# Performance work log

Measured on AMD Instinct MI355X. Metric: run time of the kernel, lower is better.

## Reference

```python
import jax, jax.numpy as jnp
import numpy as np

NUM_HEADS = 8
NUM_LEVELS = 4
NUM_POINTS = 8
SPATIAL_SHAPES = np.array([[92, 160], [46, 80], [23, 40], [12, 20]], dtype=np.int64)


def _bilinear_sample(val_hw, loc, Hl, Wl):
    """val_hw: (bs, heads, H*W, d); loc: (bs, nq, heads, P, 2) in [0,1].
    Matches torch grid_sample(bilinear, zeros padding, align_corners=False)
    applied to grid = 2*loc - 1, i.e. pixel coords x = loc_x*W - 0.5.
    Returns (bs, heads, nq, P, d)."""
    x = loc[..., 0] * Wl - 0.5
    y = loc[..., 1] * Hl - 0.5
    x0 = jnp.floor(x)
    y0 = jnp.floor(y)
    wx = (x - x0).transpose(0, 2, 1, 3)  # (bs, heads, nq, P)
    wy = (y - y0).transpose(0, 2, 1, 3)
    x0i = x0.astype(jnp.int32).transpose(0, 2, 1, 3)
    y0i = y0.astype(jnp.int32).transpose(0, 2, 1, 3)

    def gather(ix, iy):
        valid = ((ix >= 0) & (ix < Wl) & (iy >= 0) & (iy < Hl)).astype(val_hw.dtype)
        idx = jnp.clip(iy, 0, Hl - 1) * Wl + jnp.clip(ix, 0, Wl - 1)  # (bs,heads,nq,P)
        b, h, nq, P = idx.shape
        g = jnp.take_along_axis(val_hw, idx.reshape(b, h, nq * P, 1), axis=2)
        return g.reshape(b, h, nq, P, -1) * valid[..., None]

    return (gather(x0i, y0i) * ((1 - wx) * (1 - wy))[..., None]
            + gather(x0i + 1, y0i) * (wx * (1 - wy))[..., None]
            + gather(x0i, y0i + 1) * ((1 - wx) * wy)[..., None]
            + gather(x0i + 1, y0i + 1) * (wx * wy)[..., None])


def setup_inputs() -> dict:
    key = jax.random.key(0)
    ks = jax.random.split(key, 10)
    C = 256
    bs, nq = 2, 10000
    nv = int((SPATIAL_SHAPES[:, 0] * SPATIAL_SHAPES[:, 1]).sum())  # 19560
    s = 1.0 / np.sqrt(C)
    return {
        "query": jax.random.normal(ks[0], (bs, nq, C), dtype=jnp.float32),
        "value": jax.random.normal(ks[1], (bs, nv, C), dtype=jnp.float32),
        "reference_points": jax.random.uniform(ks[2], (bs, nq, 4, 2), dtype=jnp.float32),
        "spatial_shapes": SPATIAL_SHAPES,
        "W_value": jax.random.normal(ks[3], (C, C), dtype=jnp.float32) * s,
        "b_value": jnp.zeros((C,), dtype=jnp.float32),
        "W_off": jax.random.normal(ks[4], (C, NUM_HEADS * NUM_LEVELS * NUM_POINTS * 2), dtype=jnp.float32) * 0.01,
        "b_off": jax.random.normal(ks[5], (NUM_HEADS * NUM_LEVELS * NUM_POINTS * 2,), dtype=jnp.float32) * 0.1,
        "W_attn": jax.random.normal(ks[6], (C, NUM_HEADS * NUM_LEVELS * NUM_POINTS), dtype=jnp.float32) * s,
        "b_attn": jnp.zeros((NUM_HEADS * NUM_LEVELS * NUM_POINTS,), dtype=jnp.float32),
    }


def reference(query, value, reference_points, spatial_shapes,
              W_value, b_value, W_off, b_off, W_attn, b_attn):
    bs, nq, C = query.shape
    NH, NL, NP = NUM_HEADS, NUM_LEVELS, NUM_POINTS
    d = C // NH
    Z = reference_points.shape[2]  # num_Z_anchors
    shapes_np = np.asarray(spatial_shapes)  # static host-side shapes

    # value / offset / attention projections
    v = (value @ W_value + b_value).reshape(bs, -1, NH, d)
    off = (query @ W_off + b_off).reshape(bs, nq, NH, NL, NP, 2)
    attn = jax.nn.softmax((query @ W_attn + b_attn).reshape(bs, nq, NH, NL * NP), axis=-1)
    attn = attn.reshape(bs, nq, NH, NL, NP)

    # normalize offsets by (W, H) per level and add to reference points
    norm = jnp.stack([spatial_shapes[:, 1], spatial_shapes[:, 0]], -1).astype(query.dtype)  # (NL, 2)
    off = off / norm[None, None, None, :, None, :]
    off = off.reshape(bs, nq, NH, NL, NP // Z, Z, 2)
    loc = reference_points[:, :, None, None, None, :, :] + off  # (bs,nq,NH,NL,NP//Z,Z,2)
    loc = loc.reshape(bs, nq, NH, NL, NP, 2)

    out = jnp.zeros((bs, NH, nq, d), dtype=query.dtype)
    start = 0
    for l in range(NL):
        Hl, Wl = int(shapes_np[l, 0]), int(shapes_np[l, 1])
        v_l = v[:, start:start + Hl * Wl].transpose(0, 2, 1, 3)  # (bs, NH, H*W, d)
        start += Hl * Wl
        sampled = _bilinear_sample(v_l, loc[:, :, :, l], Hl, Wl)  # (bs,NH,nq,NP,d)
        out = out + jnp.einsum('bhqpd,bqhp->bhqd', sampled, attn[:, :, :, l])
    return out.transpose(0, 2, 1, 3).reshape(bs, nq, NH * d)
```

## Files before the change

### kernel.cpp

```cpp
#include <hip/hip_runtime.h>
#include <math.h>

#define NH 8
#define NL 4
#define NP 8
#define CDIM 256
#define NQ 10000
#define BS 2
#define NV 19560

__constant__ int LVL_H[NL]     = {92, 46, 23, 12};
__constant__ int LVL_W[NL]     = {160, 80, 40, 20};
__constant__ int LVL_START[NL] = {0, 14720, 18400, 19320};

typedef __attribute__((ext_vector_type(8))) short short8;
typedef __attribute__((ext_vector_type(4))) float f32x4;
typedef __attribute__((ext_vector_type(2))) _Float16 half2v;
typedef __attribute__((ext_vector_type(4))) _Float16 half4v;

__device__ __forceinline__ unsigned short f2bf(float f) {
    unsigned int u = __float_as_uint(f);
    u += 0x7fffu + ((u >> 16) & 1u);
    return (unsigned short)(u >> 16);
}

__device__ __forceinline__ unsigned cvt_pk_bf16(float lo, float hi) {
    unsigned r;
    asm("v_cvt_pk_bf16_f32 %0, %1, %2" : "=v"(r) : "v"(lo), "v"(hi));
    return r;
}

__device__ __forceinline__ unsigned f2h_dup(float f) {
    const unsigned short h = __builtin_bit_cast(unsigned short, (_Float16)f);
    return (unsigned)h | ((unsigned)h << 16);
}

__device__ __forceinline__ void glds16(const void* g, void* l) {
    __builtin_amdgcn_global_load_lds(
        (const __attribute__((address_space(1))) unsigned*)g,
        (__attribute__((address_space(3))) unsigned*)l, 16, 0, 0);
}

__global__ __launch_bounds__(256) void prep_all(
    const float* __restrict__ query,
    const float* __restrict__ Wv,
    const float* __restrict__ Woff, const float* __restrict__ boff,
    const float* __restrict__ Wattn, const float* __restrict__ battn,
    unsigned short* __restrict__ querybf,
    unsigned short* __restrict__ BvalT, unsigned short* __restrict__ BcatT,
    float* __restrict__ biascat)
{
    const int bid = blockIdx.x;
    const int t   = threadIdx.x;
    if (bid < 5000) {
        const int i = bid * 256 + t;
        const float4 f = ((const float4*)query)[i];
        ushort4 o;
        o.x = f2bf(f.x); o.y = f2bf(f.y); o.z = f2bf(f.z); o.w = f2bf(f.w);
        ((ushort4*)querybf)[i] = o;
    } else {
        const int n = bid - 5000;
        if (n < 256) {
            BvalT[n * 256 + t] = f2bf(Wv[t * 256 + n]);
        } else if (n < 1024) {
            const int m = n - 256;
            const float v = (m < 512) ? Woff[t * 512 + m]
                                      : Wattn[t * 256 + (m - 512)];
            BcatT[m * 256 + t] = f2bf(v);
        } else {
            #pragma unroll
            for (int s = 0; s < 3; s++) {
                const int i = s * 256 + t;
                biascat[i] = (i < 512) ? boff[i] : battn[i - 512];
            }
        }
    }
}

__global__ __launch_bounds__(256) void gemm_all(
    const float* __restrict__ valueF,
    const unsigned short* __restrict__ BvalT,
    const float* __restrict__ b_value, _Float16* __restrict__ vproj,
    const unsigned short* __restrict__ querybf,
    const unsigned short* __restrict__ BcatT,
    const float* __restrict__ biascat, _Float16* __restrict__ offcat)
{
    __shared__ short8 Asl[512];
    __shared__ short8 Bsl[512];

    const int bid = blockIdx.x;
    const bool modeV = bid < 612;

    const unsigned short* Bt;
    const float* bias;
    int M, N, rowBase, colBase;
    if (modeV) {
        Bt = BvalT; bias = b_value;
        M = BS * NV; N = 256;
        rowBase = (bid >> 1) * 128; colBase = (bid & 1) * 128;
    } else {
        const int b2 = bid - 612;
        Bt = BcatT; bias = biascat;
        M = BS * NQ; N = 768;
        rowBase = (b2 / 6) * 128; colBase = (b2 % 6) * 128;
    }

    const int t = threadIdx.x;
    const int w  = t >> 6;
    const int l  = t & 63;
    const int wm = (w >> 1) * 64;
    const int wn = (w & 1) * 64;
    const int row16 = l & 15;
    const int kg    = l >> 4;

    const int r0 = t >> 2;
    const int m_ = t & 3;
    const int cs = (m_ - (r0 >> 1)) & 3;

    short8* aw0 = &Asl[(w << 6)];
    short8* aw1 = &Asl[256 + (w << 6)];
    short8* bw0 = &Bsl[(w << 6)];
    short8* bw1 = &Bsl[256 + (w << 6)];

    const int arow0 = min(rowBase + r0, M - 1);
    const int arow1 = min(rowBase + r0 + 64, M - 1);
    const int brow0 = colBase + r0;
    const int brow1 = brow0 + 64;

    f32x4 acc[4][4] = {};

    for (int k0 = 0; k0 < 256; k0 += 32) {
        const int kc = k0 + cs * 8;
        glds16(Bt + (size_t)brow0 * 256 + kc, bw0);
        glds16(Bt + (size_t)brow1 * 256 + kc, bw1);
        if (modeV) {
            #pragma unroll
            for (int jj = 0; jj < 2; jj++) {
                const int ar = jj ? arow1 : arow0;
                const float* ap = valueF + (size_t)ar * 256 + kc;
                const float4 f0 = *(const float4*)ap;
                const float4 f1 = *(const float4*)(ap + 4);
                uint4 pk;
                pk.x = cvt_pk_bf16(f0.x, f0.y);
                pk.y = cvt_pk_bf16(f0.z, f0.w);
                pk.z = cvt_pk_bf16(f1.x, f1.y);
                pk.w = cvt_pk_bf16(f1.z, f1.w);
                Asl[jj * 256 + t] = __builtin_bit_cast(short8, pk);
            }
        } else {
            glds16(querybf + (size_t)arow0 * 256 + kc, aw0);
            glds16(querybf + (size_t)arow1 * 256 + kc, aw1);
        }
        __syncthreads();

        short8 af[4], bfr[4];
        #pragma unroll
        for (int i = 0; i < 4; i++) {
            const int r = wm + i * 16 + row16;
            af[i] = Asl[r * 4 + ((kg + (r >> 1)) & 3)];
        }
        #pragma unroll
        for (int j = 0; j < 4; j++) {
            const int r = wn + j * 16 + row16;
            bfr[j] = Bsl[r * 4 + ((kg + (r >> 1)) & 3)];
        }
        #pragma unroll
        for (int i = 0; i < 4; i++)
            #pragma unroll
            for (int j = 0; j < 4; j++)
                acc[i][j] = __builtin_amdgcn_mfma_f32_16x16x32_bf16(
                    bfr[j], af[i], acc[i][j], 0, 0, 0);
        __syncthreads();
    }

    const int m16 = l & 15;
    const int q4  = (l >> 4) * 4;
    #pragma unroll
    for (int i = 0; i < 4; i++) {
        const int row = rowBase + wm + i * 16 + m16;
        if (row >= M) continue;
        #pragma unroll
        for (int j = 0; j < 4; j++) {
            const int col0 = colBase + wn + j * 16 + q4;
            const float4 bv = *(const float4*)&bias[col0];
            half4v o;
            o[0] = (_Float16)(acc[i][j][0] + bv.x);
            o[1] = (_Float16)(acc[i][j][1] + bv.y);
            o[2] = (_Float16)(acc[i][j][2] + bv.z);
            o[3] = (_Float16)(acc[i][j][3] + bv.w);
            _Float16* dst;
            if (modeV) {
                const int b   = (row >= NV) ? 1 : 0;
                const int pix = row - b * NV;
                const int h   = col0 >> 5;
                const int ch  = col0 & 31;
                dst = vproj + ((size_t)(b * NH + h) * NV + pix) * 32 + ch;
            } else {
                dst = offcat + (size_t)row * 768 + col0;
            }
            *(half4v*)dst = o;
        }
    }
}

__global__ __launch_bounds__(256, 8) void sample_kernel(
    const _Float16* __restrict__ vproj,
    const _Float16* __restrict__ offcat,
    const float* __restrict__ refpts,
    float* __restrict__ out)
{
    const int bid = blockIdx.x;
    const int h   = bid & 7;
    const int g   = bid >> 3;
    const int b   = g & 1;
    const int q0  = (g >> 1) * 8;
    const int t   = threadIdx.x;

    __shared__ uint2 desc[8 * 144];

    const int qi = t >> 5, j = t & 31;
    const int qrow = b * NQ + q0 + qi;

    {
        const int lv = j >> 3, p = j & 7;

        const float logit = (float)offcat[(size_t)qrow * 768 + 512 + h * 32 + j];
        const float e = __expf(logit);
        float ssum = e;
        #pragma unroll
        for (int s = 16; s > 0; s >>= 1) ssum += __shfl_xor(ssum, s, 32);
        const float aw = e / ssum;

        const int Wl = LVL_W[lv], Hl = LVL_H[lv], st = LVL_START[lv];
        const uint oxy = *(const uint*)(offcat + (size_t)qrow * 768 + h * 64 + j * 2);
        const float offx = (float)__builtin_bit_cast(half2v, oxy)[0];
        const float offy = (float)__builtin_bit_cast(half2v, oxy)[1];

        const int z = p & 3;
        const float rx = refpts[((size_t)qrow * 4 + z) * 2];
        const float ry = refpts[((size_t)qrow * 4 + z) * 2 + 1];

        const float x = fmaf(rx, (float)Wl, offx) - 0.5f;
        const float y = fmaf(ry, (float)Hl, offy) - 0.5f;
        const float x0f = floorf(x), y0f = floorf(y);
        const float wx = x - x0f, wy = y - y0f;
        const int x0 = (int)x0f, y0 = (int)y0f;

        const int xb = min(max(x0, 0), Wl - 2);
        const float wl = (x0 >= 0 && x0 < Wl)          ? (1.f - wx) : 0.f;
        const float wr = (x0 + 1 >= 0 && x0 + 1 < Wl)  ? wx         : 0.f;
        const float wA = (x0 == xb) ? wl : ((x0 + 1 == xb) ? wr : 0.f);
        const float wB = (x0 == xb) ? wr : ((x0 == xb + 1) ? wl : 0.f);

        const int i16 = j >> 1;
        const int gA0 = qi * 144 + (((j & 1) * 2) * 2) * 18 + i16;

        #pragma unroll
        for (int r = 0; r < 2; r++) {
            const int yy = y0 + r;
            const float rwv = (yy >= 0 && yy < Hl)
                            ? (r ? wy : (1.f - wy)) * aw : 0.f;
            const int iy = min(max(yy, 0), Hl - 1);
            const unsigned base = (unsigned)((st + iy * Wl + xb) * 64);
            const int gb = gA0 + r * 2 * 18;
            desc[gb]      = make_uint2(base,      f2h_dup(wA * rwv));
            desc[gb + 18] = make_uint2(base + 64, f2h_dup(wB * rwv));
        }
    }
    __syncthreads();

    const int lane = t & 31;
    const int grp  = lane >> 3;
    const int pix  = (lane >> 2) & 1;
    const int chq  = lane & 3;

    const char* slab = (const char*)(vproj + (size_t)(b * NH + h) * NV * 32);
    const unsigned laneoff = (unsigned)(chq * 16);
    const uint4* dp = (const uint4*)&desc[qi * 144 + (grp * 2 + pix) * 18];

    half2v a0 = {}, a1 = {}, a2 = {}, a3 = {};
    #pragma unroll
    for (int half = 0; half < 2; half++) {
        uint4 d4[4];
        #pragma unroll
        for (int u2 = 0; u2 < 4; u2++) d4[u2] = dp[half * 4 + u2];
        uint4 v[8];
        #pragma unroll
        for (int u2 = 0; u2 < 4; u2++) {
            v[u2 * 2]     = *(const uint4*)(slab + (d4[u2].x + laneoff));
            v[u2 * 2 + 1] = *(const uint4*)(slab + (d4[u2].z + laneoff));
        }
        __builtin_amdgcn_sched_barrier(0);
        #pragma unroll
        for (int u2 = 0; u2 < 4; u2++) {
            const half2v w0 = __builtin_bit_cast(half2v, d4[u2].y);
            a0 += w0 * __builtin_bit_cast(half2v, v[u2 * 2].x);
            a1 += w0 * __builtin_bit_cast(half2v, v[u2 * 2].y);
            a2 += w0 * __builtin_bit_cast(half2v, v[u2 * 2].z);
            a3 += w0 * __builtin_bit_cast(half2v, v[u2 * 2].w);
            const half2v w1 = __builtin_bit_cast(half2v, d4[u2].w);
            a0 += w1 * __builtin_bit_cast(half2v, v[u2 * 2 + 1].x);
            a1 += w1 * __builtin_bit_cast(half2v, v[u2 * 2 + 1].y);
            a2 += w1 * __builtin_bit_cast(half2v, v[u2 * 2 + 1].z);
            a3 += w1 * __builtin_bit_cast(half2v, v[u2 * 2 + 1].w);
        }
    }

    #pragma unroll
    for (int s = 4; s <= 16; s <<= 1) {
        a0 += __builtin_bit_cast(half2v,
              __shfl_xor(__builtin_bit_cast(unsigned, a0), s, 32));
        a1 += __builtin_bit_cast(half2v,
              __shfl_xor(__builtin_bit_cast(unsigned, a1), s, 32));
        a2 += __builtin_bit_cast(half2v,
              __shfl_xor(__builtin_bit_cast(unsigned, a2), s, 32));
        a3 += __builtin_bit_cast(half2v,
              __shfl_xor(__builtin_bit_cast(unsigned, a3), s, 32));
    }

    if ((lane & 0x1C) == 0) {
        float* op = out + (size_t)qrow * 256 + h * 32 + chq * 8;
        *(float4*)op = make_float4((float)a0[0], (float)a0[1],
                                   (float)a1[0], (float)a1[1]);
        *(float4*)(op + 4) = make_float4((float)a2[0], (float)a2[1],
                                         (float)a3[0], (float)a3[1]);
    }
}

extern "C" void kernel_launch(void* const* d_in, const int* in_sizes, int n_in,
                              void* d_out, int out_size, void* d_ws, size_t ws_size,
                              hipStream_t stream)
{
    const float* query   = (const float*)d_in[0];
    const float* value   = (const float*)d_in[1];
    const float* refpts  = (const float*)d_in[2];
    const float* W_value = (const float*)d_in[4];
    const float* b_value = (const float*)d_in[5];
    const float* W_off   = (const float*)d_in[6];
    const float* b_off   = (const float*)d_in[7];
    const float* W_attn  = (const float*)d_in[8];
    const float* b_attn  = (const float*)d_in[9];

    char* ws = (char*)d_ws;
    _Float16*       vproj   = (_Float16*)(ws);
    unsigned short* querybf = (unsigned short*)(ws + 20029440);
    _Float16*       offcat  = (_Float16*)(ws + 30269440);
    unsigned short* BvalT   = (unsigned short*)(ws + 60989440);
    unsigned short* BcatT   = (unsigned short*)(ws + 61120512);
    float*          biascat = (float*)(ws + 61513728);

    const dim3 blk(256);

    prep_all<<<dim3(6025), blk, 0, stream>>>(
        query, W_value, W_off, b_off, W_attn, b_attn,
        querybf, BvalT, BcatT, biascat);

    gemm_all<<<dim3(1554), blk, 0, stream>>>(
        value, BvalT, b_value, vproj,
        querybf, BcatT, biascat, offcat);

    sample_kernel<<<dim3(BS * NQ), blk, 0, stream>>>(
        vproj, offcat, refpts, (float*)d_out);
}
```

Before: 211.9 us.

## Double-buffer GEMM LDS tiles, remap blocks across XCDs, relax sample occupancy

The fused GEMM kernel now double-buffers its A and B shared-memory tiles, issuing the next k-step's global-to-LDS loads before computing on the current tile. It replaces __syncthreads with explicit waitcnt plus s_barrier so loads overlap with MFMA work. Block IDs are remapped so that consecutive logical tiles land on the same XCD, improving L2 reuse. The sample kernel's launch bound drops from 8 to 6 blocks per CU, which allows more registers per thread. The hand-written vmcnt counts are fragile and could cause races if the compiler's ordering of memory operations differs from what they assume.

```diff
diff --git a/kernel.cpp b/kernel.cpp
--- a/kernel.cpp
+++ b/kernel.cpp
@@ -85,10 +85,15 @@
     const unsigned short* __restrict__ BcatT,
     const float* __restrict__ biascat, _Float16* __restrict__ offcat)
 {
-    __shared__ short8 Asl[512];
-    __shared__ short8 Bsl[512];
-
-    const int bid = blockIdx.x;
+    __shared__ short8 Asl[2][512];
+    __shared__ short8 Bsl[2][512];
+
+    const int orig = blockIdx.x;
+    const int xcd  = orig & 7, lid = orig >> 3;
+    const int q_   = 1554 >> 3, r_ = 1554 & 7;
+    const int bid  = (xcd < r_ ? xcd * (q_ + 1)
+                               : r_ * (q_ + 1) + (xcd - r_) * q_) + lid;
+
     const bool modeV = bid < 612;
 
     const unsigned short* Bt;
@@ -117,10 +122,7 @@
     const int m_ = t & 3;
     const int cs = (m_ - (r0 >> 1)) & 3;
 
-    short8* aw0 = &Asl[(w << 6)];
-    short8* aw1 = &Asl[256 + (w << 6)];
-    short8* bw0 = &Bsl[(w << 6)];
-    short8* bw1 = &Bsl[256 + (w << 6)];
+    const int wb = w << 6;
 
     const int arow0 = min(rowBase + r0, M - 1);
     const int arow1 = min(rowBase + r0 + 64, M - 1);
@@ -129,40 +131,62 @@
 
     f32x4 acc[4][4] = {};
 
-    for (int k0 = 0; k0 < 256; k0 += 32) {
-        const int kc = k0 + cs * 8;
-        glds16(Bt + (size_t)brow0 * 256 + kc, bw0);
-        glds16(Bt + (size_t)brow1 * 256 + kc, bw1);
+    #define STAGE_Q(s, p) do {                                            \
+        const int kc = (s) * 32 + cs * 8;                                 \
+        glds16(querybf + (size_t)arow0 * 256 + kc, &Asl[p][wb]);          \
+        glds16(querybf + (size_t)arow1 * 256 + kc, &Asl[p][256 + wb]);    \
+        glds16(Bt + (size_t)brow0 * 256 + kc, &Bsl[p][wb]);               \
+        glds16(Bt + (size_t)brow1 * 256 + kc, &Bsl[p][256 + wb]);         \
+    } while (0)
+
+    #define STAGE_V(s, p) do {                                            \
+        const int kc = (s) * 32 + cs * 8;                                 \
+        const float* a0p = valueF + (size_t)arow0 * 256 + kc;             \
+        const float* a1p = valueF + (size_t)arow1 * 256 + kc;             \
+        const float4 f00 = *(const float4*)a0p;                           \
+        const float4 f01 = *(const float4*)(a0p + 4);                     \
+        const float4 f10 = *(const float4*)a1p;                           \
+        const float4 f11 = *(const float4*)(a1p + 4);                     \
+        glds16(Bt + (size_t)brow0 * 256 + kc, &Bsl[p][wb]);               \
+        glds16(Bt + (size_t)brow1 * 256 + kc, &Bsl[p][256 + wb]);         \
+        uint4 pk0, pk1;                                                   \
+        pk0.x = cvt_pk_bf16(f00.x, f00.y); pk0.y = cvt_pk_bf16(f00.z, f00.w); \
+        pk0.z = cvt_pk_bf16(f01.x, f01.y); pk0.w = cvt_pk_bf16(f01.z, f01.w); \
+        pk1.x = cvt_pk_bf16(f10.x, f10.y); pk1.y = cvt_pk_bf16(f10.z, f10.w); \
+        pk1.z = cvt_pk_bf16(f11.x, f11.y); pk1.w = cvt_pk_bf16(f11.z, f11.w); \
+        Asl[p][t]       = __builtin_bit_cast(short8, pk0);                \
+        Asl[p][256 + t] = __builtin_bit_cast(short8, pk1);                \
+    } while (0)
+
+    if (modeV) STAGE_V(0, 0); else STAGE_Q(0, 0);
+
+    for (int ts = 0; ts < 8; ++ts) {
+        const int cur = ts & 1;
+        if (ts < 7) {
+            if (modeV) STAGE_V(ts + 1, cur ^ 1);
+            else       STAGE_Q(ts + 1, cur ^ 1);
+        }
         if (modeV) {
-            #pragma unroll
-            for (int jj = 0; jj < 2; jj++) {
-                const int ar = jj ? arow1 : arow0;
-                const float* ap = valueF + (size_t)ar * 256 + kc;
-                const float4 f0 = *(const float4*)ap;
-                const float4 f1 = *(const float4*)(ap + 4);
-                uint4 pk;
-                pk.x = cvt_pk_bf16(f0.x, f0.y);
-                pk.y = cvt_pk_bf16(f0.z, f0.w);
-                pk.z = cvt_pk_bf16(f1.x, f1.y);
-                pk.w = cvt_pk_bf16(f1.z, f1.w);
-                Asl[jj * 256 + t] = __builtin_bit_cast(short8, pk);
-            }
+            if (ts < 7) asm volatile("s_waitcnt lgkmcnt(0)" ::: "memory");
+            else        asm volatile("s_waitcnt vmcnt(0) lgkmcnt(0)" ::: "memory");
         } else {
-            glds16(querybf + (size_t)arow0 * 256 + kc, aw0);
-            glds16(querybf + (size_t)arow1 * 256 + kc, aw1);
-        }
-        __syncthreads();
+            if (ts < 7) asm volatile("s_waitcnt vmcnt(4)" ::: "memory");
+            else        asm volatile("s_waitcnt vmcnt(0)" ::: "memory");
+        }
+        __builtin_amdgcn_sched_barrier(0);
+        __builtin_amdgcn_s_barrier();
+        __builtin_amdgcn_sched_barrier(0);
 
         short8 af[4], bfr[4];
         #pragma unroll
         for (int i = 0; i < 4; i++) {
             const int r = wm + i * 16 + row16;
-            af[i] = Asl[r * 4 + ((kg + (r >> 1)) & 3)];
+            af[i] = Asl[cur][r * 4 + ((kg + (r >> 1)) & 3)];
         }
         #pragma unroll
         for (int j = 0; j < 4; j++) {
             const int r = wn + j * 16 + row16;
-            bfr[j] = Bsl[r * 4 + ((kg + (r >> 1)) & 3)];
+            bfr[j] = Bsl[cur][r * 4 + ((kg + (r >> 1)) & 3)];
         }
         #pragma unroll
         for (int i = 0; i < 4; i++)
@@ -170,8 +194,12 @@
             for (int j = 0; j < 4; j++)
                 acc[i][j] = __builtin_amdgcn_mfma_f32_16x16x32_bf16(
                     bfr[j], af[i], acc[i][j], 0, 0, 0);
-        __syncthreads();
-    }
+
+        __builtin_amdgcn_s_barrier();
+        __builtin_amdgcn_sched_barrier(0);
+    }
+    #undef STAGE_Q
+    #undef STAGE_V
 
     const int m16 = l & 15;
     const int q4  = (l >> 4) * 4;
@@ -203,7 +231,7 @@
     }
 }
 
-__global__ __launch_bounds__(256, 8) void sample_kernel(
+__global__ __launch_bounds__(256, 6) void sample_kernel(
     const _Float16* __restrict__ vproj,
     const _Float16* __restrict__ offcat,
     const float* __restrict__ refpts,
```

Measured after the change: 205.0 us. -3.2%, faster.
